# Performance work log

Hardware: AMD Instinct MI355X
Metric: run time of the kernel (lower is better)

## Reference

```python
import jax, jax.numpy as jnp
import numpy as np

D_MODEL = 1024
D_STATE = 16
D_CONV = 4
EXPAND = 2
D_INNER = EXPAND * D_MODEL  # 2048
DT_RANK = 64
B, L = 1, 1024


def setup_inputs() -> dict:
    key = jax.random.key(0)
    ks = jax.random.split(key, 10)
    s = 0.02
    x = jax.random.normal(ks[0], (B, L, D_MODEL), dtype=jnp.float32)
    in_proj_w = jax.random.normal(ks[1], (2 * D_INNER, D_MODEL), dtype=jnp.float32) * s
    conv_w = jax.random.normal(ks[2], (D_INNER, 1, D_CONV), dtype=jnp.float32) * s
    conv_b = jax.random.normal(ks[3], (D_INNER,), dtype=jnp.float32) * s
    x_proj_w = jax.random.normal(ks[4], (DT_RANK + 2 * D_STATE, D_INNER), dtype=jnp.float32) * s
    dt_init_std = DT_RANK ** (-0.5)
    dt_proj_w = jax.random.uniform(ks[5], (D_INNER, DT_RANK), dtype=jnp.float32,
                                   minval=-dt_init_std, maxval=dt_init_std)
    dt = jnp.exp(jax.random.uniform(ks[6], (D_INNER,), dtype=jnp.float32)
                 * (np.log(0.1) - np.log(0.001)) + np.log(0.001))
    dt = jnp.clip(dt, 1e-4, None)
    dt_proj_b = dt + jnp.log(-jnp.expm1(-dt))  # inverse softplus
    A_log = jnp.log(jnp.broadcast_to(jnp.arange(1, D_STATE + 1, dtype=jnp.float32),
                                     (D_INNER, D_STATE)))
    D = jnp.ones((D_INNER,), dtype=jnp.float32)
    out_proj_w = jax.random.normal(ks[7], (D_MODEL, D_INNER), dtype=jnp.float32) * s
    return {"x": x, "in_proj_w": in_proj_w, "conv_w": conv_w, "conv_b": conv_b,
            "x_proj_w": x_proj_w, "dt_proj_w": dt_proj_w, "dt_proj_b": dt_proj_b,
            "A_log": A_log, "D": D, "out_proj_w": out_proj_w}


def _selective_scan(u, delta, A, Bm, Cm, Dv):
    # u, delta: [b,l,d]; A: [d,n]; Bm, Cm: [b,l,n]; Dv: [d]
    deltaA = jnp.exp(jnp.einsum('bld,dn->bldn', delta, A))           # [b,l,d,n]
    deltaB_u = jnp.einsum('bld,bld,bln->bldn', delta, u, Bm)          # [b,l,d,n]
    xs = (jnp.swapaxes(deltaA, 0, 1), jnp.swapaxes(deltaB_u, 0, 1),
          jnp.swapaxes(Cm, 0, 1))  # time-major

    def step(state, inp):
        dA_t, dBu_t, C_t = inp               # [b,d,n], [b,d,n], [b,n]
        state = dA_t * state + dBu_t
        y_t = jnp.einsum('bdn,bn->bd', state, C_t)
        return state, y_t

    state0 = jnp.zeros((u.shape[0], u.shape[2], A.shape[1]), dtype=u.dtype)
    _, ys = jax.lax.scan(step, state0, xs)    # ys: [l,b,d]
    y = jnp.swapaxes(ys, 0, 1)
    return y + u * Dv


def reference(x, in_proj_w, conv_w, conv_b, x_proj_w, dt_proj_w, dt_proj_b,
              A_log, D, out_proj_w):
    b, l, _ = x.shape
    xz = x @ in_proj_w.T                      # [b,l,2*d_inner]
    xi, z = jnp.split(xz, 2, axis=-1)
    # causal depthwise conv1d (pad left d_conv-1, truncate to L)
    xc = jnp.swapaxes(xi, 1, 2)               # [b,d_inner,l]
    xc = jax.lax.conv_general_dilated(
        xc, conv_w, window_strides=(1,), padding=[(D_CONV - 1, 0)],
        dimension_numbers=('NCH', 'OIH', 'NCH'), feature_group_count=D_INNER)
    xc = xc + conv_b[None, :, None]
    xi = jax.nn.silu(jnp.swapaxes(xc, 1, 2))  # [b,l,d_inner]
    # SSM
    A = -jnp.exp(A_log)
    x_dbl = xi @ x_proj_w.T                   # [b,l,dt_rank+2n]
    delta, Bm, Cm = jnp.split(x_dbl, [DT_RANK, DT_RANK + D_STATE], axis=-1)
    delta = jax.nn.softplus(delta @ dt_proj_w.T + dt_proj_b)
    y = _selective_scan(xi, delta, A, Bm, Cm, D)
    y = y * jax.nn.silu(z)
    return y @ out_proj_w.T
```

## Files before the change

kernel.cpp:

```cpp
#include <hip/hip_runtime.h>
#include <hip/hip_bf16.h>
#include <cstdint>
#include <cstddef>


typedef __attribute__((ext_vector_type(4))) float f32x4;
typedef __attribute__((ext_vector_type(8))) short short8;

#define GLOAD_LDS16(g, l)                                                      \
  __builtin_amdgcn_global_load_lds(                                            \
      (const __attribute__((address_space(1))) void*)(g),                      \
      (__attribute__((address_space(3))) void*)(l), 16, 0, 0)

__device__ __forceinline__ unsigned short f2bf(float f) {
  union { float f; unsigned u; } v; v.f = f;
  unsigned u = v.u;
  unsigned r = (u + 0x7FFFu + ((u >> 16) & 1u)) >> 16;
  return (unsigned short)r;
}
__device__ __forceinline__ float bf2f(unsigned short u) {
  union { unsigned u; float f; } v; v.u = ((unsigned)u) << 16;
  return v.f;
}

__global__ __launch_bounds__(256) void convert_all(
    const float* __restrict__ a0, unsigned short* __restrict__ o0, int n0,
    const float* __restrict__ a1, unsigned short* __restrict__ o1, int n1,
    const float* __restrict__ a2, unsigned short* __restrict__ o2, int n2,
    const float* __restrict__ a3, unsigned short* __restrict__ o3, int n3,
    const float* __restrict__ a4, unsigned short* __restrict__ o4, int n4) {
  const float* a; unsigned short* o; int n;
  switch (blockIdx.y) {
    case 0: a = a0; o = o0; n = n0; break;
    case 1: a = a1; o = o1; n = n1; break;
    case 2: a = a2; o = o2; n = n2; break;
    case 3: a = a3; o = o3; n = n3; break;
    default: a = a4; o = o4; n = n4; break;
  }
  int n4c = n >> 2;
  int stride = gridDim.x * blockDim.x;
  for (int i = blockIdx.x * blockDim.x + threadIdx.x; i < n4c; i += stride) {
    float4 v = ((const float4*)a)[i];
    uint2 p;
    p.x = (unsigned)f2bf(v.x) | ((unsigned)f2bf(v.y) << 16);
    p.y = (unsigned)f2bf(v.z) | ((unsigned)f2bf(v.w) << 16);
    ((uint2*)o)[i] = p;
  }
}

template <int SPLITK, int OBF>
__global__ __launch_bounds__(256) void gemm64(
    const unsigned short* __restrict__ A, const unsigned short* __restrict__ B,
    void* __restrict__ Cv, int M, int N, int K) {
  __shared__ unsigned short lds[2][2][64 * 64];
  const int tid  = threadIdx.x;
  const int lane = tid & 63;
  const int w    = tid >> 6;

  const int nx = gridDim.x, ny = gridDim.y;
  int l = (blockIdx.z * ny + blockIdx.y) * nx + blockIdx.x;
  int xcd = l & 7, idx = l >> 3;
  int by = idx % ny;
  int r_ = idx / ny;
  int slab = nx >> 3;
  int bx = xcd * slab + (r_ % slab);
  int bz = r_ / slab;

  const int mBase = by * 64;
  const int nBase = bx * 64;
  const int kLen  = K / SPLITK;
  const int kBase = (SPLITK > 1) ? bz * kLen : 0;
  const int wr = (w >> 1) * 32;
  const int wc = (w & 1) * 32;
  const int wchunk = tid & 192;

  f32x4 acc[2][2];
  #pragma unroll
  for (int m = 0; m < 2; ++m)
    #pragma unroll
    for (int n = 0; n < 2; ++n)
      acc[m][n] = (f32x4){0.f, 0.f, 0.f, 0.f};

  auto stage = [&](int b, int k0) {
    #pragma unroll
    for (int j = 0; j < 2; ++j) {
      int chunk = tid + j * 256;
      int row = chunk >> 3;
      int t = chunk & 7;
      int col = (t ^ (row & 7)) * 8;
      GLOAD_LDS16(&A[(size_t)(mBase + row) * K + k0 + col],
                  &lds[b][0][(size_t)(wchunk + j * 256) * 8]);
      GLOAD_LDS16(&B[(size_t)(nBase + row) * K + k0 + col],
                  &lds[b][1][(size_t)(wchunk + j * 256) * 8]);
    }
  };

  const int kIters = kLen / 64;
  stage(0, kBase);
  __syncthreads();
  int buf = 0;
  for (int it = 0; it < kIters; ++it) {
    if (it + 1 < kIters) stage(buf ^ 1, kBase + (it + 1) * 64);
    short8 af[2][2], bfr[2][2];
    #pragma unroll
    for (int m = 0; m < 2; ++m)
      #pragma unroll
      for (int kk = 0; kk < 2; ++kk) {
        int row = wr + m * 16 + (lane & 15);
        int s = kk * 4 + (lane >> 4);
        af[m][kk] = *(const short8*)&lds[buf][0][row * 64 + ((s ^ (row & 7)) * 8)];
      }
    #pragma unroll
    for (int n = 0; n < 2; ++n)
      #pragma unroll
      for (int kk = 0; kk < 2; ++kk) {
        int row = wc + n * 16 + (lane & 15);
        int s = kk * 4 + (lane >> 4);
        bfr[n][kk] = *(const short8*)&lds[buf][1][row * 64 + ((s ^ (row & 7)) * 8)];
      }
    #pragma unroll
    for (int kk = 0; kk < 2; ++kk)
      #pragma unroll
      for (int m = 0; m < 2; ++m)
        #pragma unroll
        for (int n = 0; n < 2; ++n)
          acc[m][n] = __builtin_amdgcn_mfma_f32_16x16x32_bf16(
              af[m][kk], bfr[n][kk], acc[m][n], 0, 0, 0);
    __syncthreads();
    buf ^= 1;
  }

  if (OBF) {
    unsigned short* Cb = (unsigned short*)Cv;
    #pragma unroll
    for (int m = 0; m < 2; ++m) {
      int row0 = mBase + wr + m * 16 + (lane >> 4) * 4;
      #pragma unroll
      for (int n = 0; n < 2; ++n) {
        int col = nBase + wc + n * 16 + (lane & 15);
        #pragma unroll
        for (int r = 0; r < 4; ++r)
          Cb[(size_t)(row0 + r) * N + col] = f2bf(acc[m][n][r]);
      }
    }
  } else {
    float* Co = (float*)Cv + (SPLITK > 1 ? (size_t)bz * M * N : (size_t)0);
    #pragma unroll
    for (int m = 0; m < 2; ++m) {
      int row0 = mBase + wr + m * 16 + (lane >> 4) * 4;
      #pragma unroll
      for (int n = 0; n < 2; ++n) {
        int col = nBase + wc + n * 16 + (lane & 15);
        #pragma unroll
        for (int r = 0; r < 4; ++r)
          Co[(size_t)(row0 + r) * N + col] = acc[m][n][r];
      }
    }
  }
}

__global__ __launch_bounds__(256) void reduce2(
    const float* __restrict__ P, float* __restrict__ out, int n4) {
  int i = blockIdx.x * 256 + threadIdx.x;
  if (i < n4) {
    f32x4 a = ((const f32x4*)P)[i];
    f32x4 b = ((const f32x4*)P)[i + n4];
    ((f32x4*)out)[i] = a + b;
  }
}

__global__ __launch_bounds__(256) void conv_silu(
    const unsigned short* __restrict__ xz_bf, const float* __restrict__ cw,
    const float* __restrict__ cb, unsigned short* __restrict__ xi_b) {
  int d0 = threadIdx.x * 8;
  int l0 = blockIdx.x * 4;
  float wgt[8][4], bias[8];
  #pragma unroll
  for (int j = 0; j < 8; ++j) {
    float4 t = *(const float4*)&cw[(d0 + j) * 4];
    wgt[j][0] = t.x; wgt[j][1] = t.y; wgt[j][2] = t.z; wgt[j][3] = t.w;
  }
  *(float4*)(bias + 0) = *(const float4*)&cb[d0];
  *(float4*)(bias + 4) = *(const float4*)&cb[d0 + 4];

  short8 rows[7];
  #pragma unroll
  for (int r = 0; r < 7; ++r) {
    int ll = l0 - 3 + r;
    if (ll >= 0)
      rows[r] = *(const short8*)&xz_bf[(size_t)ll * 4096 + d0];
    else
      rows[r] = (short8){0, 0, 0, 0, 0, 0, 0, 0};
  }
  #pragma unroll
  for (int q = 0; q < 4; ++q) {
    short8 outv;
    #pragma unroll
    for (int j = 0; j < 8; ++j) {
      float acc = bias[j];
      #pragma unroll
      for (int k = 0; k < 4; ++k)
        acc = fmaf(bf2f((unsigned short)rows[q + k][j]), wgt[j][k], acc);
      float s = acc / (1.f + __expf(-acc));
      outv[j] = (short)f2bf(s);
    }
    *(short8*)&xi_b[(size_t)(l0 + q) * 2048 + d0] = outv;
  }
}

__global__ __launch_bounds__(256) void xproj(
    const unsigned short* __restrict__ xi_b, const unsigned short* __restrict__ xw_b,
    unsigned short* __restrict__ xd_b, float* __restrict__ Bm, float* __restrict__ Cm) {
  __shared__ f32x4 red[4][64];
  int tid = threadIdx.x, lane = tid & 63, w = tid >> 6;
  int mt = blockIdx.x, nt = blockIdx.y;
  int arow = mt * 16 + (lane & 15);
  int brow = nt * 16 + (lane & 15);
  int kg = (lane >> 4) * 8;
  f32x4 acc = (f32x4){0.f, 0.f, 0.f, 0.f};
  for (int k0 = w * 512; k0 < (w + 1) * 512; k0 += 32) {
    short8 a = *(const short8*)&xi_b[(size_t)arow * 2048 + k0 + kg];
    short8 b = *(const short8*)&xw_b[(size_t)brow * 2048 + k0 + kg];
    acc = __builtin_amdgcn_mfma_f32_16x16x32_bf16(a, b, acc, 0, 0, 0);
  }
  red[w][lane] = acc;
  __syncthreads();
  if (w == 0) {
    acc = red[0][lane];
    acc += red[1][lane];
    acc += red[2][lane];
    acc += red[3][lane];
    int ocol = nt * 16 + (lane & 15);
    #pragma unroll
    for (int r = 0; r < 4; ++r) {
      int row = mt * 16 + (lane >> 4) * 4 + r;
      float v = acc[r];
      if (ocol < 64)      xd_b[row * 64 + ocol] = f2bf(v);
      else if (ocol < 80) Bm[row * 16 + (ocol - 64)] = v;
      else                Cm[row * 16 + (ocol - 80)] = v;
    }
  }
}

__global__ __launch_bounds__(64) void dtproj(
    const unsigned short* __restrict__ xd_b, const unsigned short* __restrict__ dtw_b,
    const float* __restrict__ dtb, float* __restrict__ delta) {
  int lane = threadIdx.x;
  int mt = blockIdx.x, nt = blockIdx.y;
  int arow = mt * 16 + (lane & 15);
  int brow = nt * 16 + (lane & 15);
  int kg = (lane >> 4) * 8;
  f32x4 acc = (f32x4){0.f, 0.f, 0.f, 0.f};
  #pragma unroll
  for (int k0 = 0; k0 < 64; k0 += 32) {
    short8 a = *(const short8*)&xd_b[arow * 64 + k0 + kg];
    short8 b = *(const short8*)&dtw_b[brow * 64 + k0 + kg];
    acc = __builtin_amdgcn_mfma_f32_16x16x32_bf16(a, b, acc, 0, 0, 0);
  }
  int ocol = nt * 16 + (lane & 15);
  float bias = dtb[ocol];
  #pragma unroll
  for (int r = 0; r < 4; ++r) {
    int row = mt * 16 + (lane >> 4) * 4 + r;
    float v = acc[r] + bias;
    float sp = (v > 20.f) ? v : log1pf(__expf(v));
    delta[(size_t)row * 2048 + ocol] = sp;
  }
}

__global__ __launch_bounds__(64) void scan_p1(
    const float* __restrict__ delta, const unsigned short* __restrict__ xi_b,
    const float* __restrict__ Bm, const float* __restrict__ A_log,
    float* __restrict__ P, float* __restrict__ S) {
  int d = blockIdx.x * 64 + threadIdx.x;
  int c = blockIdx.y;
  float a[16], p[16], s[16];
  #pragma unroll
  for (int n = 0; n < 16; ++n) {
    a[n] = -__expf(A_log[d * 16 + n]);
    p[n] = 1.f; s[n] = 0.f;
  }
  for (int tb = 0; tb < 8; ++tb) {
    int l0 = c * 32 + tb * 4;
    float dl[4], uu[4], bv[4][16];
    #pragma unroll
    for (int q = 0; q < 4; ++q) {
      dl[q] = delta[(size_t)(l0 + q) * 2048 + d];
      uu[q] = bf2f(xi_b[(size_t)(l0 + q) * 2048 + d]);
      *(float4*)(bv[q] + 0)  = *(const float4*)&Bm[(l0 + q) * 16 + 0];
      *(float4*)(bv[q] + 4)  = *(const float4*)&Bm[(l0 + q) * 16 + 4];
      *(float4*)(bv[q] + 8)  = *(const float4*)&Bm[(l0 + q) * 16 + 8];
      *(float4*)(bv[q] + 12) = *(const float4*)&Bm[(l0 + q) * 16 + 12];
    }
    #pragma unroll
    for (int q = 0; q < 4; ++q) {
      float du = dl[q] * uu[q];
      #pragma unroll
      for (int n = 0; n < 16; ++n) {
        float dA = __expf(dl[q] * a[n]);
        s[n] = fmaf(dA, s[n], du * bv[q][n]);
        p[n] *= dA;
      }
    }
  }
  #pragma unroll
  for (int n = 0; n < 16; ++n) {
    P[(size_t)(c * 16 + n) * 2048 + d] = p[n];
    S[(size_t)(c * 16 + n) * 2048 + d] = s[n];
  }
}

__global__ __launch_bounds__(256) void scan_p2(
    const float* __restrict__ P, const float* __restrict__ S,
    float* __restrict__ SIn) {
  int idx = blockIdx.x * 256 + threadIdx.x;
  float sin_ = 0.f;
  #pragma unroll 8
  for (int c = 0; c < 32; ++c) {
    SIn[c * 32768 + idx] = sin_;
    sin_ = fmaf(P[c * 32768 + idx], sin_, S[c * 32768 + idx]);
  }
}

__global__ __launch_bounds__(64) void scan_p3(
    const float* __restrict__ delta, const unsigned short* __restrict__ xi_b,
    const float* __restrict__ Bm, const float* __restrict__ Cm,
    const float* __restrict__ A_log, const float* __restrict__ Dv,
    const float* __restrict__ SIn, const unsigned short* __restrict__ xz_bf,
    unsigned short* __restrict__ y_b) {
  int d = blockIdx.x * 64 + threadIdx.x;
  int c = blockIdx.y;
  float a[16], s[16];
  #pragma unroll
  for (int n = 0; n < 16; ++n) {
    a[n] = -__expf(A_log[d * 16 + n]);
    s[n] = SIn[c * 32768 + n * 2048 + d];
  }
  float Dd = Dv[d];
  for (int tb = 0; tb < 16; ++tb) {
    int l0 = c * 32 + tb * 2;
    float dl[2], uu[2], zz[2], bv[2][16], cv[2][16];
    #pragma unroll
    for (int q = 0; q < 2; ++q) {
      int l = l0 + q;
      dl[q] = delta[(size_t)l * 2048 + d];
      uu[q] = bf2f(xi_b[(size_t)l * 2048 + d]);
      zz[q] = bf2f(xz_bf[(size_t)l * 4096 + 2048 + d]);
      *(float4*)(bv[q] + 0)  = *(const float4*)&Bm[l * 16 + 0];
      *(float4*)(bv[q] + 4)  = *(const float4*)&Bm[l * 16 + 4];
      *(float4*)(bv[q] + 8)  = *(const float4*)&Bm[l * 16 + 8];
      *(float4*)(bv[q] + 12) = *(const float4*)&Bm[l * 16 + 12];
      *(float4*)(cv[q] + 0)  = *(const float4*)&Cm[l * 16 + 0];
      *(float4*)(cv[q] + 4)  = *(const float4*)&Cm[l * 16 + 4];
      *(float4*)(cv[q] + 8)  = *(const float4*)&Cm[l * 16 + 8];
      *(float4*)(cv[q] + 12) = *(const float4*)&Cm[l * 16 + 12];
    }
    #pragma unroll
    for (int q = 0; q < 2; ++q) {
      float du = dl[q] * uu[q];
      float y = 0.f;
      #pragma unroll
      for (int n = 0; n < 16; ++n) {
        float dA = __expf(dl[q] * a[n]);
        s[n] = fmaf(dA, s[n], du * bv[q][n]);
        y = fmaf(s[n], cv[q][n], y);
      }
      y = fmaf(uu[q], Dd, y);
      float sig = 1.f / (1.f + __expf(-zz[q]));
      y *= zz[q] * sig;
      y_b[(size_t)(l0 + q) * 2048 + d] = f2bf(y);
    }
  }
}

extern "C" void kernel_launch(void* const* d_in, const int* in_sizes, int n_in,
                              void* d_out, int out_size, void* d_ws, size_t ws_size,
                              hipStream_t stream) {
  const float* x      = (const float*)d_in[0];
  const float* Win    = (const float*)d_in[1];
  const float* convw  = (const float*)d_in[2];
  const float* convb  = (const float*)d_in[3];
  const float* xprojw = (const float*)d_in[4];
  const float* dtw    = (const float*)d_in[5];
  const float* dtb    = (const float*)d_in[6];
  const float* Alog   = (const float*)d_in[7];
  const float* Dv     = (const float*)d_in[8];
  const float* Wout   = (const float*)d_in[9];
  float* out = (float*)d_out;

  char* ws = (char*)d_ws;
  size_t off = 0;
  auto alloc = [&](size_t bytes) -> void* {
    void* p = ws + off;
    off = (off + bytes + 255) & ~(size_t)255;
    return p;
  };
  unsigned short* x_bf    = (unsigned short*)alloc((size_t)1024 * 1024 * 2);
  unsigned short* Win_bf  = (unsigned short*)alloc((size_t)4096 * 1024 * 2);
  unsigned short* Wout_bf = (unsigned short*)alloc((size_t)1024 * 2048 * 2);
  unsigned short* xw_bf   = (unsigned short*)alloc((size_t)96 * 2048 * 2);
  unsigned short* dtw_bf  = (unsigned short*)alloc((size_t)2048 * 64 * 2);
  unsigned short* xz_bf   = (unsigned short*)alloc((size_t)1024 * 4096 * 2);
  unsigned short* xi_bf   = (unsigned short*)alloc((size_t)1024 * 2048 * 2);
  unsigned short* xd_bf   = (unsigned short*)alloc((size_t)1024 * 64 * 2);
  float* Bm               = (float*)alloc((size_t)1024 * 16 * 4);
  float* Cm               = (float*)alloc((size_t)1024 * 16 * 4);
  float* delta            = (float*)alloc((size_t)1024 * 2048 * 4);
  float* P                = (float*)alloc((size_t)32 * 16 * 2048 * 4);
  float* S                = (float*)alloc((size_t)32 * 16 * 2048 * 4);
  float* SIn              = (float*)alloc((size_t)32 * 16 * 2048 * 4);
  unsigned short* y_bf    = (unsigned short*)alloc((size_t)1024 * 2048 * 2);

  convert_all<<<dim3(512, 5), 256, 0, stream>>>(
      x, x_bf, 1024 * 1024,
      Win, Win_bf, 4096 * 1024,
      Wout, Wout_bf, 1024 * 2048,
      xprojw, xw_bf, 96 * 2048,
      dtw, dtw_bf, 2048 * 64);
  gemm64<1, 1><<<dim3(64, 16), 256, 0, stream>>>(x_bf, Win_bf, xz_bf, 1024, 4096, 1024);
  conv_silu<<<dim3(256), 256, 0, stream>>>(xz_bf, convw, convb, xi_bf);
  xproj<<<dim3(64, 6), 256, 0, stream>>>(xi_bf, xw_bf, xd_bf, Bm, Cm);
  dtproj<<<dim3(64, 128), 64, 0, stream>>>(xd_bf, dtw_bf, dtb, delta);
  scan_p1<<<dim3(32, 32), 64, 0, stream>>>(delta, xi_bf, Bm, Alog, P, S);
  scan_p2<<<dim3(128), 256, 0, stream>>>(P, S, SIn);
  scan_p3<<<dim3(32, 32), 64, 0, stream>>>(delta, xi_bf, Bm, Cm, Alog, Dv, SIn, xz_bf, y_bf);
  gemm64<2, 0><<<dim3(16, 16, 2), 256, 0, stream>>>(y_bf, Wout_bf, P, 1024, 1024, 2048);
  reduce2<<<dim3(1024), 256, 0, stream>>>(P, out, 262144);
}
```

Measured before the change: 109.6 us.

## Fuse dt projection and three-phase scan into one cooperative kernel

Replaces the dtproj, scan_p1, scan_p2 and scan_p3 kernels with a single cooperative kernel. Each block computes its delta tile with MFMA straight into LDS and keeps u, B and C there, so the full delta tensor is never written to or re-read from global memory. The inter-chunk prefix runs between two grid-wide syncs. This removes three launches and the delta traffic, but relies on all 1024 blocks being co-resident and adds grid-sync cost.

```diff
diff --git a/kernel.cpp b/kernel.cpp
--- a/kernel.cpp
+++ b/kernel.cpp
@@ -1,8 +1,11 @@
 #include <hip/hip_runtime.h>
 #include <hip/hip_bf16.h>
+#include <hip/hip_cooperative_groups.h>
 #include <cstdint>
 #include <cstddef>
 
+
+namespace cg = cooperative_groups;
 
 typedef __attribute__((ext_vector_type(4))) float f32x4;
 typedef __attribute__((ext_vector_type(8))) short short8;
@@ -242,65 +245,97 @@
   }
 }
 
-__global__ __launch_bounds__(64) void dtproj(
-    const unsigned short* __restrict__ xd_b, const unsigned short* __restrict__ dtw_b,
-    const float* __restrict__ dtb, float* __restrict__ delta) {
-  int lane = threadIdx.x;
-  int mt = blockIdx.x, nt = blockIdx.y;
-  int arow = mt * 16 + (lane & 15);
-  int brow = nt * 16 + (lane & 15);
-  int kg = (lane >> 4) * 8;
-  f32x4 acc = (f32x4){0.f, 0.f, 0.f, 0.f};
-  #pragma unroll
-  for (int k0 = 0; k0 < 64; k0 += 32) {
-    short8 a = *(const short8*)&xd_b[arow * 64 + k0 + kg];
-    short8 b = *(const short8*)&dtw_b[brow * 64 + k0 + kg];
-    acc = __builtin_amdgcn_mfma_f32_16x16x32_bf16(a, b, acc, 0, 0, 0);
-  }
-  int ocol = nt * 16 + (lane & 15);
-  float bias = dtb[ocol];
-  #pragma unroll
-  for (int r = 0; r < 4; ++r) {
-    int row = mt * 16 + (lane >> 4) * 4 + r;
-    float v = acc[r] + bias;
-    float sp = (v > 20.f) ? v : log1pf(__expf(v));
-    delta[(size_t)row * 2048 + ocol] = sp;
-  }
-}
-
-__global__ __launch_bounds__(64) void scan_p1(
-    const float* __restrict__ delta, const unsigned short* __restrict__ xi_b,
-    const float* __restrict__ Bm, const float* __restrict__ A_log,
-    float* __restrict__ P, float* __restrict__ S) {
-  int d = blockIdx.x * 64 + threadIdx.x;
-  int c = blockIdx.y;
+__global__ __launch_bounds__(64) void scan_fused(
+    const unsigned short* __restrict__ xd, const unsigned short* __restrict__ dtw,
+    const float* __restrict__ dtb, const unsigned short* __restrict__ xi,
+    const float* __restrict__ BmG, const float* __restrict__ CmG,
+    const float* __restrict__ Alog, const float* __restrict__ Dv,
+    const unsigned short* __restrict__ xz, float* __restrict__ P,
+    float* __restrict__ S, float* __restrict__ SIn,
+    unsigned short* __restrict__ y_b) {
+  __shared__ float ldsD[32 * 64];
+  __shared__ unsigned short ldsU[32 * 64];
+  __shared__ float ldsB[32 * 16];
+  __shared__ float ldsC[32 * 16];
+  const int bid = blockIdx.x;
+  const int dblk = bid & 31, c = bid >> 5;
+  const int lane = threadIdx.x;
+  const int d = dblk * 64 + lane;
+
+  #pragma unroll
+  for (int i = 0; i < 8; ++i) {
+    ldsB[lane + i * 64] = BmG[c * 512 + lane + i * 64];
+    ldsC[lane + i * 64] = CmG[c * 512 + lane + i * 64];
+  }
+
+  {
+    short8 afr[2][2], bfr[4][2];
+    #pragma unroll
+    for (int lt = 0; lt < 2; ++lt)
+      #pragma unroll
+      for (int kk = 0; kk < 2; ++kk)
+        afr[lt][kk] = *(const short8*)
+            &xd[(size_t)(c * 32 + lt * 16 + (lane & 15)) * 64 + kk * 32 + (lane >> 4) * 8];
+    #pragma unroll
+    for (int dt = 0; dt < 4; ++dt)
+      #pragma unroll
+      for (int kk = 0; kk < 2; ++kk)
+        bfr[dt][kk] = *(const short8*)
+            &dtw[(size_t)(dblk * 64 + dt * 16 + (lane & 15)) * 64 + kk * 32 + (lane >> 4) * 8];
+    f32x4 acc[2][4];
+    #pragma unroll
+    for (int lt = 0; lt < 2; ++lt)
+      #pragma unroll
+      for (int dt = 0; dt < 4; ++dt)
+        acc[lt][dt] = (f32x4){0.f, 0.f, 0.f, 0.f};
+    #pragma unroll
+    for (int kk = 0; kk < 2; ++kk)
+      #pragma unroll
+      for (int lt = 0; lt < 2; ++lt)
+        #pragma unroll
+        for (int dt = 0; dt < 4; ++dt)
+          acc[lt][dt] = __builtin_amdgcn_mfma_f32_16x16x32_bf16(
+              afr[lt][kk], bfr[dt][kk], acc[lt][dt], 0, 0, 0);
+    #pragma unroll
+    for (int dt = 0; dt < 4; ++dt) {
+      int dl_ = dt * 16 + (lane & 15);
+      float bias = dtb[dblk * 64 + dl_];
+      #pragma unroll
+      for (int lt = 0; lt < 2; ++lt) {
+        #pragma unroll
+        for (int r = 0; r < 4; ++r) {
+          int ll = lt * 16 + (lane >> 4) * 4 + r;
+          float v = acc[lt][dt][r] + bias;
+          float sp = (v > 20.f) ? v : log1pf(__expf(v));
+          ldsD[ll * 64 + dl_] = sp;
+        }
+      }
+    }
+  }
+
   float a[16], p[16], s[16];
   #pragma unroll
   for (int n = 0; n < 16; ++n) {
-    a[n] = -__expf(A_log[d * 16 + n]);
+    a[n] = -__expf(Alog[d * 16 + n]);
     p[n] = 1.f; s[n] = 0.f;
   }
-  for (int tb = 0; tb < 8; ++tb) {
-    int l0 = c * 32 + tb * 4;
-    float dl[4], uu[4], bv[4][16];
-    #pragma unroll
-    for (int q = 0; q < 4; ++q) {
-      dl[q] = delta[(size_t)(l0 + q) * 2048 + d];
-      uu[q] = bf2f(xi_b[(size_t)(l0 + q) * 2048 + d]);
-      *(float4*)(bv[q] + 0)  = *(const float4*)&Bm[(l0 + q) * 16 + 0];
-      *(float4*)(bv[q] + 4)  = *(const float4*)&Bm[(l0 + q) * 16 + 4];
-      *(float4*)(bv[q] + 8)  = *(const float4*)&Bm[(l0 + q) * 16 + 8];
-      *(float4*)(bv[q] + 12) = *(const float4*)&Bm[(l0 + q) * 16 + 12];
-    }
-    #pragma unroll
-    for (int q = 0; q < 4; ++q) {
-      float du = dl[q] * uu[q];
-      #pragma unroll
-      for (int n = 0; n < 16; ++n) {
-        float dA = __expf(dl[q] * a[n]);
-        s[n] = fmaf(dA, s[n], du * bv[q][n]);
-        p[n] *= dA;
-      }
+  for (int t = 0; t < 32; ++t) {
+    int l = c * 32 + t;
+    float dl = ldsD[t * 64 + lane];
+    unsigned short ub = xi[(size_t)l * 2048 + d];
+    ldsU[t * 64 + lane] = ub;
+    float u = bf2f(ub);
+    float du = dl * u;
+    float bv[16];
+    *(float4*)(bv + 0)  = *(const float4*)&ldsB[t * 16 + 0];
+    *(float4*)(bv + 4)  = *(const float4*)&ldsB[t * 16 + 4];
+    *(float4*)(bv + 8)  = *(const float4*)&ldsB[t * 16 + 8];
+    *(float4*)(bv + 12) = *(const float4*)&ldsB[t * 16 + 12];
+    #pragma unroll
+    for (int n = 0; n < 16; ++n) {
+      float dA = __expf(dl * a[n]);
+      s[n] = fmaf(dA, s[n], du * bv[n]);
+      p[n] *= dA;
     }
   }
   #pragma unroll
@@ -308,68 +343,53 @@
     P[(size_t)(c * 16 + n) * 2048 + d] = p[n];
     S[(size_t)(c * 16 + n) * 2048 + d] = s[n];
   }
-}
-
-__global__ __launch_bounds__(256) void scan_p2(
-    const float* __restrict__ P, const float* __restrict__ S,
-    float* __restrict__ SIn) {
-  int idx = blockIdx.x * 256 + threadIdx.x;
-  float sin_ = 0.f;
-  #pragma unroll 8
-  for (int c = 0; c < 32; ++c) {
-    SIn[c * 32768 + idx] = sin_;
-    sin_ = fmaf(P[c * 32768 + idx], sin_, S[c * 32768 + idx]);
-  }
-}
-
-__global__ __launch_bounds__(64) void scan_p3(
-    const float* __restrict__ delta, const unsigned short* __restrict__ xi_b,
-    const float* __restrict__ Bm, const float* __restrict__ Cm,
-    const float* __restrict__ A_log, const float* __restrict__ Dv,
-    const float* __restrict__ SIn, const unsigned short* __restrict__ xz_bf,
-    unsigned short* __restrict__ y_b) {
-  int d = blockIdx.x * 64 + threadIdx.x;
-  int c = blockIdx.y;
-  float a[16], s[16];
-  #pragma unroll
-  for (int n = 0; n < 16; ++n) {
-    a[n] = -__expf(A_log[d * 16 + n]);
+
+  __threadfence();
+  cg::this_grid().sync();
+
+  int gid = bid * 64 + lane;
+  if (gid < 32768) {
+    float run = 0.f;
+    #pragma unroll 4
+    for (int cc = 0; cc < 32; ++cc) {
+      SIn[cc * 32768 + gid] = run;
+      run = fmaf(P[cc * 32768 + gid], run, S[cc * 32768 + gid]);
+    }
+  }
+
+  __threadfence();
+  cg::this_grid().sync();
+
+  #pragma unroll
+  for (int n = 0; n < 16; ++n)
     s[n] = SIn[c * 32768 + n * 2048 + d];
-  }
   float Dd = Dv[d];
-  for (int tb = 0; tb < 16; ++tb) {
-    int l0 = c * 32 + tb * 2;
-    float dl[2], uu[2], zz[2], bv[2][16], cv[2][16];
-    #pragma unroll
-    for (int q = 0; q < 2; ++q) {
-      int l = l0 + q;
-      dl[q] = delta[(size_t)l * 2048 + d];
-      uu[q] = bf2f(xi_b[(size_t)l * 2048 + d]);
-      zz[q] = bf2f(xz_bf[(size_t)l * 4096 + 2048 + d]);
-      *(float4*)(bv[q] + 0)  = *(const float4*)&Bm[l * 16 + 0];
-      *(float4*)(bv[q] + 4)  = *(const float4*)&Bm[l * 16 + 4];
-      *(float4*)(bv[q] + 8)  = *(const float4*)&Bm[l * 16 + 8];
-      *(float4*)(bv[q] + 12) = *(const float4*)&Bm[l * 16 + 12];
-      *(float4*)(cv[q] + 0)  = *(const float4*)&Cm[l * 16 + 0];
-      *(float4*)(cv[q] + 4)  = *(const float4*)&Cm[l * 16 + 4];
-      *(float4*)(cv[q] + 8)  = *(const float4*)&Cm[l * 16 + 8];
-      *(float4*)(cv[q] + 12) = *(const float4*)&Cm[l * 16 + 12];
-    }
-    #pragma unroll
-    for (int q = 0; q < 2; ++q) {
-      float du = dl[q] * uu[q];
-      float y = 0.f;
-      #pragma unroll
-      for (int n = 0; n < 16; ++n) {
-        float dA = __expf(dl[q] * a[n]);
-        s[n] = fmaf(dA, s[n], du * bv[q][n]);
-        y = fmaf(s[n], cv[q][n], y);
-      }
-      y = fmaf(uu[q], Dd, y);
-      float sig = 1.f / (1.f + __expf(-zz[q]));
-      y *= zz[q] * sig;
-      y_b[(size_t)(l0 + q) * 2048 + d] = f2bf(y);
-    }
+  for (int t = 0; t < 32; ++t) {
+    int l = c * 32 + t;
+    float dl = ldsD[t * 64 + lane];
+    float u  = bf2f(ldsU[t * 64 + lane]);
+    float du = dl * u;
+    float bv[16], cv[16];
+    *(float4*)(bv + 0)  = *(const float4*)&ldsB[t * 16 + 0];
+    *(float4*)(bv + 4)  = *(const float4*)&ldsB[t * 16 + 4];
+    *(float4*)(bv + 8)  = *(const float4*)&ldsB[t * 16 + 8];
+    *(float4*)(bv + 12) = *(const float4*)&ldsB[t * 16 + 12];
+    *(float4*)(cv + 0)  = *(const float4*)&ldsC[t * 16 + 0];
+    *(float4*)(cv + 4)  = *(const float4*)&ldsC[t * 16 + 4];
+    *(float4*)(cv + 8)  = *(const float4*)&ldsC[t * 16 + 8];
+    *(float4*)(cv + 12) = *(const float4*)&ldsC[t * 16 + 12];
+    float y = 0.f;
+    #pragma unroll
+    for (int n = 0; n < 16; ++n) {
+      float dA = __expf(dl * a[n]);
+      s[n] = fmaf(dA, s[n], du * bv[n]);
+      y = fmaf(s[n], cv[n], y);
+    }
+    y = fmaf(u, Dd, y);
+    float zz = bf2f(xz[(size_t)l * 4096 + 2048 + d]);
+    float sig = 1.f / (1.f + __expf(-zz));
+    y *= zz * sig;
+    y_b[(size_t)l * 2048 + d] = f2bf(y);
   }
 }
 
@@ -405,7 +425,6 @@
   unsigned short* xd_bf   = (unsigned short*)alloc((size_t)1024 * 64 * 2);
   float* Bm               = (float*)alloc((size_t)1024 * 16 * 4);
   float* Cm               = (float*)alloc((size_t)1024 * 16 * 4);
-  float* delta            = (float*)alloc((size_t)1024 * 2048 * 4);
   float* P                = (float*)alloc((size_t)32 * 16 * 2048 * 4);
   float* S                = (float*)alloc((size_t)32 * 16 * 2048 * 4);
   float* SIn              = (float*)alloc((size_t)32 * 16 * 2048 * 4);
@@ -420,10 +439,17 @@
   gemm64<1, 1><<<dim3(64, 16), 256, 0, stream>>>(x_bf, Win_bf, xz_bf, 1024, 4096, 1024);
   conv_silu<<<dim3(256), 256, 0, stream>>>(xz_bf, convw, convb, xi_bf);
   xproj<<<dim3(64, 6), 256, 0, stream>>>(xi_bf, xw_bf, xd_bf, Bm, Cm);
-  dtproj<<<dim3(64, 128), 64, 0, stream>>>(xd_bf, dtw_bf, dtb, delta);
-  scan_p1<<<dim3(32, 32), 64, 0, stream>>>(delta, xi_bf, Bm, Alog, P, S);
-  scan_p2<<<dim3(128), 256, 0, stream>>>(P, S, SIn);
-  scan_p3<<<dim3(32, 32), 64, 0, stream>>>(delta, xi_bf, Bm, Cm, Alog, Dv, SIn, xz_bf, y_bf);
+
+  {
+    void* args[] = {
+      (void*)&xd_bf, (void*)&dtw_bf, (void*)&dtb, (void*)&xi_bf,
+      (void*)&Bm, (void*)&Cm, (void*)&Alog, (void*)&Dv,
+      (void*)&xz_bf, (void*)&P, (void*)&S, (void*)&SIn, (void*)&y_bf
+    };
+    hipLaunchCooperativeKernel((const void*)scan_fused, dim3(1024), dim3(64),
+                               args, 0, stream);
+  }
+
   gemm64<2, 0><<<dim3(16, 16, 2), 256, 0, stream>>>(y_bf, Wout_bf, P, 1024, 1024, 2048);
   reduce2<<<dim3(1024), 256, 0, stream>>>(P, out, 262144);
 }
```

Result: slower. 360.0 us (+228.6%).

## Replace LDS-staged GEMM with direct-from-global MFMA GEMM and split-K by four

Applied to the files above, without the earlier changes.

Removes LDS staging and double buffering from the GEMM. Each wave now loads its MFMA fragments straight from global memory, relying on the caches for reuse, and the tile width becomes a template parameter. The in_proj GEMM uses a 64x128 tile with half as many blocks. The out_proj GEMM moves from split-K 2 to split-K 4 with a new 4-way reduction buffer, trading extra partial-sum traffic for more blocks and no barriers. It risks uncoalesced, poorly reused global loads compared with the shared-memory tiles.

```diff
diff --git a/kernel.cpp b/kernel.cpp
--- a/kernel.cpp
+++ b/kernel.cpp
@@ -6,11 +6,6 @@
 
 typedef __attribute__((ext_vector_type(4))) float f32x4;
 typedef __attribute__((ext_vector_type(8))) short short8;
-
-#define GLOAD_LDS16(g, l)                                                      \
-  __builtin_amdgcn_global_load_lds(                                            \
-      (const __attribute__((address_space(1))) void*)(g),                      \
-      (__attribute__((address_space(3))) void*)(l), 16, 0, 0)
 
 __device__ __forceinline__ unsigned short f2bf(float f) {
   union { float f; unsigned u; } v; v.f = f;
@@ -48,18 +43,17 @@
   }
 }
 
-template <int SPLITK, int OBF>
-__global__ __launch_bounds__(256) void gemm64(
+template <int FN, int SPLITK, int OBF>
+__global__ __launch_bounds__(256) void gemm_direct(
     const unsigned short* __restrict__ A, const unsigned short* __restrict__ B,
     void* __restrict__ Cv, int M, int N, int K) {
-  __shared__ unsigned short lds[2][2][64 * 64];
   const int tid  = threadIdx.x;
   const int lane = tid & 63;
   const int w    = tid >> 6;
 
   const int nx = gridDim.x, ny = gridDim.y;
-  int l = (blockIdx.z * ny + blockIdx.y) * nx + blockIdx.x;
-  int xcd = l & 7, idx = l >> 3;
+  int li = (blockIdx.z * ny + blockIdx.y) * nx + blockIdx.x;
+  int xcd = li & 7, idx = li >> 3;
   int by = idx % ny;
   int r_ = idx / ny;
   int slab = nx >> 3;
@@ -67,67 +61,39 @@
   int bz = r_ / slab;
 
   const int mBase = by * 64;
-  const int nBase = bx * 64;
+  const int nBase = bx * (32 * FN);
   const int kLen  = K / SPLITK;
   const int kBase = (SPLITK > 1) ? bz * kLen : 0;
   const int wr = (w >> 1) * 32;
-  const int wc = (w & 1) * 32;
-  const int wchunk = tid & 192;
-
-  f32x4 acc[2][2];
+  const int wc = (w & 1) * (16 * FN);
+
+  const unsigned short* pa = A + (size_t)(mBase + wr + (lane & 15)) * K
+                               + kBase + (lane >> 4) * 8;
+  const unsigned short* pb = B + (size_t)(nBase + wc + (lane & 15)) * K
+                               + kBase + (lane >> 4) * 8;
+
+  f32x4 acc[2][FN];
   #pragma unroll
   for (int m = 0; m < 2; ++m)
     #pragma unroll
-    for (int n = 0; n < 2; ++n)
+    for (int n = 0; n < FN; ++n)
       acc[m][n] = (f32x4){0.f, 0.f, 0.f, 0.f};
 
-  auto stage = [&](int b, int k0) {
-    #pragma unroll
-    for (int j = 0; j < 2; ++j) {
-      int chunk = tid + j * 256;
-      int row = chunk >> 3;
-      int t = chunk & 7;
-      int col = (t ^ (row & 7)) * 8;
-      GLOAD_LDS16(&A[(size_t)(mBase + row) * K + k0 + col],
-                  &lds[b][0][(size_t)(wchunk + j * 256) * 8]);
-      GLOAD_LDS16(&B[(size_t)(nBase + row) * K + k0 + col],
-                  &lds[b][1][(size_t)(wchunk + j * 256) * 8]);
-    }
-  };
-
-  const int kIters = kLen / 64;
-  stage(0, kBase);
-  __syncthreads();
-  int buf = 0;
-  for (int it = 0; it < kIters; ++it) {
-    if (it + 1 < kIters) stage(buf ^ 1, kBase + (it + 1) * 64);
-    short8 af[2][2], bfr[2][2];
+  #pragma unroll 4
+  for (int k0 = 0; k0 < kLen; k0 += 32) {
+    short8 af[2], bf[FN];
     #pragma unroll
     for (int m = 0; m < 2; ++m)
-      #pragma unroll
-      for (int kk = 0; kk < 2; ++kk) {
-        int row = wr + m * 16 + (lane & 15);
-        int s = kk * 4 + (lane >> 4);
-        af[m][kk] = *(const short8*)&lds[buf][0][row * 64 + ((s ^ (row & 7)) * 8)];
-      }
-    #pragma unroll
-    for (int n = 0; n < 2; ++n)
-      #pragma unroll
-      for (int kk = 0; kk < 2; ++kk) {
-        int row = wc + n * 16 + (lane & 15);
-        int s = kk * 4 + (lane >> 4);
-        bfr[n][kk] = *(const short8*)&lds[buf][1][row * 64 + ((s ^ (row & 7)) * 8)];
-      }
-    #pragma unroll
-    for (int kk = 0; kk < 2; ++kk)
-      #pragma unroll
-      for (int m = 0; m < 2; ++m)
-        #pragma unroll
-        for (int n = 0; n < 2; ++n)
-          acc[m][n] = __builtin_amdgcn_mfma_f32_16x16x32_bf16(
-              af[m][kk], bfr[n][kk], acc[m][n], 0, 0, 0);
-    __syncthreads();
-    buf ^= 1;
+      af[m] = *(const short8*)(pa + (size_t)m * 16 * K + k0);
+    #pragma unroll
+    for (int n = 0; n < FN; ++n)
+      bf[n] = *(const short8*)(pb + (size_t)n * 16 * K + k0);
+    #pragma unroll
+    for (int m = 0; m < 2; ++m)
+      #pragma unroll
+      for (int n = 0; n < FN; ++n)
+        acc[m][n] = __builtin_amdgcn_mfma_f32_16x16x32_bf16(
+            af[m], bf[n], acc[m][n], 0, 0, 0);
   }
 
   if (OBF) {
@@ -136,7 +102,7 @@
     for (int m = 0; m < 2; ++m) {
       int row0 = mBase + wr + m * 16 + (lane >> 4) * 4;
       #pragma unroll
-      for (int n = 0; n < 2; ++n) {
+      for (int n = 0; n < FN; ++n) {
         int col = nBase + wc + n * 16 + (lane & 15);
         #pragma unroll
         for (int r = 0; r < 4; ++r)
@@ -149,7 +115,7 @@
     for (int m = 0; m < 2; ++m) {
       int row0 = mBase + wr + m * 16 + (lane >> 4) * 4;
       #pragma unroll
-      for (int n = 0; n < 2; ++n) {
+      for (int n = 0; n < FN; ++n) {
         int col = nBase + wc + n * 16 + (lane & 15);
         #pragma unroll
         for (int r = 0; r < 4; ++r)
@@ -159,13 +125,15 @@
   }
 }
 
-__global__ __launch_bounds__(256) void reduce2(
+__global__ __launch_bounds__(256) void reduce4(
     const float* __restrict__ P, float* __restrict__ out, int n4) {
   int i = blockIdx.x * 256 + threadIdx.x;
   if (i < n4) {
     f32x4 a = ((const f32x4*)P)[i];
     f32x4 b = ((const f32x4*)P)[i + n4];
-    ((f32x4*)out)[i] = a + b;
+    f32x4 c = ((const f32x4*)P)[i + 2 * n4];
+    f32x4 d = ((const f32x4*)P)[i + 3 * n4];
+    ((f32x4*)out)[i] = (a + b) + (c + d);
   }
 }
 
@@ -410,6 +378,7 @@
   float* S                = (float*)alloc((size_t)32 * 16 * 2048 * 4);
   float* SIn              = (float*)alloc((size_t)32 * 16 * 2048 * 4);
   unsigned short* y_bf    = (unsigned short*)alloc((size_t)1024 * 2048 * 2);
+  float* part4            = (float*)alloc((size_t)4 * 1024 * 1024 * 4);
 
   convert_all<<<dim3(512, 5), 256, 0, stream>>>(
       x, x_bf, 1024 * 1024,
@@ -417,13 +386,15 @@
       Wout, Wout_bf, 1024 * 2048,
       xprojw, xw_bf, 96 * 2048,
       dtw, dtw_bf, 2048 * 64);
-  gemm64<1, 1><<<dim3(64, 16), 256, 0, stream>>>(x_bf, Win_bf, xz_bf, 1024, 4096, 1024);
+  gemm_direct<4, 1, 1><<<dim3(32, 16), 256, 0, stream>>>(
+      x_bf, Win_bf, xz_bf, 1024, 4096, 1024);
   conv_silu<<<dim3(256), 256, 0, stream>>>(xz_bf, convw, convb, xi_bf);
   xproj<<<dim3(64, 6), 256, 0, stream>>>(xi_bf, xw_bf, xd_bf, Bm, Cm);
   dtproj<<<dim3(64, 128), 64, 0, stream>>>(xd_bf, dtw_bf, dtb, delta);
   scan_p1<<<dim3(32, 32), 64, 0, stream>>>(delta, xi_bf, Bm, Alog, P, S);
   scan_p2<<<dim3(128), 256, 0, stream>>>(P, S, SIn);
   scan_p3<<<dim3(32, 32), 64, 0, stream>>>(delta, xi_bf, Bm, Cm, Alog, Dv, SIn, xz_bf, y_bf);
-  gemm64<2, 0><<<dim3(16, 16, 2), 256, 0, stream>>>(y_bf, Wout_bf, P, 1024, 1024, 2048);
-  reduce2<<<dim3(1024), 256, 0, stream>>>(P, out, 262144);
-}
+  gemm_direct<2, 4, 0><<<dim3(16, 16, 4), 256, 0, stream>>>(
+      y_bf, Wout_bf, part4, 1024, 1024, 2048);
+  reduce4<<<dim3(1024), 256, 0, stream>>>(part4, out, 262144);
+}
```

After: 163.3 us. 1.49x slower.
